# Performance work log

Measured on AMD Instinct MI355X. Metric: run time of the kernel, lower is better.

Reference implementation:

```python
import jax, jax.numpy as jnp
import numpy as np
from math import factorial

# ---- static config mirroring Cace.__init__ ----
MAX_L = 3            # max angular degree
N_RBF = 8            # Bessel radial basis size
RB = 8               # n_radial_basis (radial embedding dim after transform)
K = 3                # n_atom_basis -> edge channels C = K*K
NZ = 4               # len(zs)
CUTOFF = 5.5
N_NODES = 2000
N_EDGES = 50000
T_MP = 1             # num_message_passing
MP_NORM = 1.0 / np.sqrt(25.0)   # 1/sqrt(avg_num_neighbors)
C = K * K

def _lxlylz(max_l):
    out = []
    for l in range(max_l + 1):
        for lx in range(l, -1, -1):
            for ly in range(l - lx, -1, -1):
                out.append((lx, ly, l - lx - ly))
    return out

L_LIST = _lxlylz(MAX_L)                 # 20 Cartesian monomials for max_l=3
NL = len(L_LIST)
LX = np.array([t[0] for t in L_LIST]); LY = np.array([t[1] for t in L_LIST]); LZ = np.array([t[2] for t in L_LIST])
DEGS = LX + LY + LZ                     # degree l of each monomial
MULTI = np.array([factorial(int(d)) / (factorial(int(a)) * factorial(int(b)) * factorial(int(c)))
                  for a, b, c, d in zip(LX, LY, LZ, DEGS)], dtype=np.float32)
SEL = np.zeros((NL, MAX_L + 1), np.float32)
SEL[np.arange(NL), DEGS] = 1.0          # monomial -> degree one-hot (for per-l sums)
NB = 1 + (MAX_L + 1)                    # symmetrizer feats: nu=1 (l=0) + nu=2 per l

def bessel(r):  # [E] -> [E, N_RBF]
    n = jnp.arange(1, N_RBF + 1, dtype=r.dtype)
    return jnp.sqrt(2.0 / CUTOFF) * jnp.sin(n[None, :] * jnp.pi * r[:, None] / CUTOFF) / r[:, None]

def poly_cutoff(r):  # MACE-style polynomial cutoff, p=6
    p = 6.0
    u = r / CUTOFF
    f = 1.0 - (p + 1.0) * (p + 2.0) / 2.0 * u**6 + p * (p + 2.0) * u**7 - p * (p + 1.0) / 2.0 * u**8
    return f * (u < 1.0)

def axis_pows(x):  # [E] -> [E, MAX_L+1] = x^0..x^MAX_L (safe grads, handles negatives)
    pows = [jnp.ones_like(x)]
    for _ in range(MAX_L):
        pows.append(pows[-1] * x)
    return jnp.stack(pows, axis=1)

def angular(u):  # unit vectors [E,3] -> Cartesian monomials [E, NL]
    return axis_pows(u[:, 0])[:, LX] * axis_pows(u[:, 1])[:, LY] * axis_pows(u[:, 2])[:, LZ]

def radial_transform(x, W):  # x [N,R,L,C], W [MAX_L+1,R,Rb] shared per degree l
    return jnp.einsum('nrlc,lrb->nblc', x, W[DEGS])

def symmetrize(A):  # A [N,Rb,NL,C] -> B [N,Rb,NB,C]
    b1 = A[:, :, :1, :]  # nu=1: the (0,0,0) monomial (index 0)
    w = (A * A) * jnp.asarray(MULTI)[None, None, :, None]
    b2 = jnp.einsum('nrlc,lm->nrmc', w, jnp.asarray(SEL))  # nu=2 invariant per degree l
    return jnp.concatenate([b1, b2], axis=2)


def setup_inputs() -> dict:
    key = jax.random.key(0)
    ks = jax.random.split(key, 9)
    positions = jax.random.uniform(ks[0], (N_NODES, 3), dtype=jnp.float32) * 12.0
    species = jax.random.randint(ks[1], (N_NODES,), 0, NZ)
    send = jax.random.randint(ks[2], (N_EDGES,), 0, N_NODES)
    off = jax.random.randint(ks[3], (N_EDGES,), 1, N_NODES)
    recv = (send + off) % N_NODES  # no self-edges -> strictly positive edge lengths
    edge_index = jnp.stack([send, recv])
    shifts = jnp.zeros((N_EDGES, 3), jnp.float32)
    W_embed = jax.random.normal(ks[4], (NZ, K), jnp.float32)
    W_radial = jax.random.normal(ks[5], (MAX_L + 1, N_RBF, RB), jnp.float32) / np.sqrt(N_RBF)
    W_mem = jax.random.normal(ks[6], (MAX_L + 1, RB, RB), jnp.float32) / np.sqrt(RB)
    W_ar = jax.random.normal(ks[7], (N_RBF, RB), jnp.float32) / np.sqrt(N_RBF)
    W_chi = jax.random.normal(ks[8], (RB, NB), jnp.float32) * 0.1
    return {"positions": positions, "shifts": shifts, "W_embed": W_embed, "W_radial": W_radial,
            "W_mem": W_mem, "W_ar": W_ar, "W_chi": W_chi, "species": species, "edge_index": edge_index}


def reference(positions, shifts, W_embed, W_radial, W_mem, W_ar, W_chi, species, edge_index):
    n_nodes = positions.shape[0]
    send, recv = edge_index[0], edge_index[1]
    # edge geometry
    vec = positions[recv] - positions[send] + shifts
    lengths = jnp.linalg.norm(vec, axis=-1)
    u = vec / (lengths[:, None] + 1e-9)
    rad = bessel(lengths)          # [E,R]
    fcut = poly_cutoff(lengths)    # [E]
    ang = angular(u)               # [E,NL]
    # edge type encoding: outer product of sender/receiver species embeddings
    emb = W_embed[species]         # [N,K]
    enc = (emb[send][:, :, None] * emb[recv][:, None, :]).reshape(-1, C)  # [E,C]
    # elementwise_multiply_3tensors -> [E,R,NL,C]
    edge_attri = jnp.einsum('er,el,ec->erlc', rad * fcut[:, None], ang, enc)
    A = radial_transform(jax.ops.segment_sum(edge_attri, recv, num_segments=n_nodes), W_radial)  # [N,Rb,NL,C]
    B = symmetrize(A)              # [N,Rb,NB,C]
    feats = [B]
    for _ in range(T_MP):
        mem = jnp.einsum('nrlc,lrb->nblc', A, W_mem[DEGS])        # NodeMemory
        chi = jnp.einsum('nbkc,bk->nc', B, W_chi)                  # MessageBchi node scalar
        msg_bchi = edge_attri * chi[send][:, None, None, :]
        A_bchi = radial_transform(jax.ops.segment_sum(msg_bchi, recv, num_segments=n_nodes), W_radial)
        fr = (rad @ W_ar) * fcut[:, None]                          # MessageAr radial filter [E,Rb]
        msg_ar = A[send] * fr[:, :, None, None]
        A_ar = jax.ops.segment_sum(msg_ar, recv, num_segments=n_nodes)
        A = (A_ar + A_bchi) * MP_NORM + mem
        B = symmetrize(A)
        feats.append(B)
    return jnp.stack(feats, axis=-1)   # [N,Rb,NB,C,T_MP+1]
```

## Files before the change

kernel.cpp:

```cpp
#include <hip/hip_runtime.h>
#include <hip/hip_bf16.h>
#include <hip/hip_cooperative_groups.h>


#define CUTF 5.5f
#define MPNORM 0.2f

namespace cg = cooperative_groups;

__constant__ int   d_DEGS[20]  = {0,1,1,1,2,2,2,2,2,2,3,3,3,3,3,3,3,3,3,3};
__constant__ float d_MULTI[20] = {1,1,1,1,1,2,2,1,2,1,1,3,3,3,6,3,1,3,3,1};

__global__ __launch_bounds__(1024) void k_prep(const int* __restrict__ eidx,
                                               int* __restrict__ offs,
                                               int* __restrict__ cursor,
                                               int N, int E) {
  __shared__ int cnt[2048];
  __shared__ int part[1024];
  int t = threadIdx.x;
  cnt[t] = 0; cnt[t + 1024] = 0;
  for (int i = t; i < N; i += 1024) cursor[i] = 0;
  __syncthreads();
  const int* recv = eidx + E;
  if ((E & 3) == 0) {
    #pragma unroll 2
    for (int i = t * 4; i + 3 < E; i += 4096) {
      int4 v = *reinterpret_cast<const int4*>(recv + i);
      atomicAdd(&cnt[v.x], 1); atomicAdd(&cnt[v.y], 1);
      atomicAdd(&cnt[v.z], 1); atomicAdd(&cnt[v.w], 1);
    }
  } else {
    #pragma unroll 4
    for (int i = t; i < E; i += 1024) atomicAdd(&cnt[recv[i]], 1);
  }
  __syncthreads();
  int a = cnt[2 * t], b = cnt[2 * t + 1];
  int s = a + b;
  part[t] = s;
  __syncthreads();
  for (int d = 1; d < 1024; d <<= 1) {
    int add = (t >= d) ? part[t - d] : 0;
    __syncthreads();
    part[t] += add;
    __syncthreads();
  }
  int excl = part[t] - s;
  if (2 * t     < N) offs[2 * t]     = excl;
  if (2 * t + 1 < N) offs[2 * t + 1] = excl + a;
  if (t == 1023) offs[N] = part[1023];
}

__global__ void k_edge(const float* __restrict__ pos,
                       const float* __restrict__ shifts,
                       const float* __restrict__ Wemb,
                       const float* __restrict__ War,
                       const int* __restrict__ species,
                       const int* __restrict__ eidx,
                       const int* __restrict__ offs,
                       int* __restrict__ cursor,
                       float* __restrict__ edata,
                       int* __restrict__ esend,
                       int E) {
  __shared__ float war_s[64];
  int t = threadIdx.x;
  if (t < 64) war_s[t] = War[t];
  __syncthreads();
  int e = blockIdx.x * blockDim.x + t;
  if (e >= E) return;
  int s  = eidx[e];
  int rI = eidx[E + e];
  float vx = pos[rI*3+0] - pos[s*3+0] + shifts[e*3+0];
  float vy = pos[rI*3+1] - pos[s*3+1] + shifts[e*3+1];
  float vz = pos[rI*3+2] - pos[s*3+2] + shifts[e*3+2];
  float len = sqrtf(vx*vx + vy*vy + vz*vz);
  float inv = 1.0f / (len + 1e-9f);
  float ux = vx*inv, uy = vy*inv, uz = vz*inv;
  float uu = len * (1.0f/CUTF);
  float u2 = uu*uu, u6 = u2*u2*u2;
  float fcut = (uu < 1.0f) ? (1.0f - 28.0f*u6 + 48.0f*u6*uu - 21.0f*u6*u2) : 0.0f;
  float x = 3.14159265358979f * uu;
  float sn = sinf(x), c2 = 2.0f*cosf(x), snm1 = 0.0f;
  float pref = sqrtf(2.0f/CUTF) / (len + 1e-20f);
  float rad[8];
  float v[48];
  #pragma unroll
  for (int k = 0; k < 8; k++) {
    rad[k] = pref * sn;
    v[k]   = rad[k] * fcut;
    float nxt = c2*sn - snm1; snm1 = sn; sn = nxt;
  }
  #pragma unroll
  for (int b = 0; b < 8; b++) {
    float a = 0.0f;
    #pragma unroll
    for (int k = 0; k < 8; k++) a += rad[k] * war_s[k*8+b];
    v[8+b] = a * fcut;
  }
  float px2 = ux*ux, py2 = uy*uy, pz2 = uz*uz;
  v[16] = 1.0f; v[17] = ux;     v[18] = uy;     v[19] = uz;
  v[20] = px2;  v[21] = ux*uy;  v[22] = ux*uz;  v[23] = py2;
  v[24] = uy*uz;v[25] = pz2;
  v[26] = px2*ux; v[27] = px2*uy; v[28] = px2*uz; v[29] = ux*py2;
  v[30] = ux*uy*uz; v[31] = ux*pz2; v[32] = py2*uy; v[33] = py2*uz;
  v[34] = uy*pz2; v[35] = pz2*uz;
  int zs = species[s], zr = species[rI];
  float es0 = Wemb[zs*3+0], es1 = Wemb[zs*3+1], es2 = Wemb[zs*3+2];
  float er0 = Wemb[zr*3+0], er1 = Wemb[zr*3+1], er2 = Wemb[zr*3+2];
  v[36] = es0*er0; v[37] = es0*er1; v[38] = es0*er2;
  v[39] = es1*er0; v[40] = es1*er1; v[41] = es1*er2;
  v[42] = es2*er0; v[43] = es2*er1; v[44] = es2*er2;
  v[45] = 0.0f; v[46] = 0.0f; v[47] = 0.0f;
  int slot = atomicAdd(&cursor[rI], 1);
  int dst = offs[rI] + slot;
  float4* eb4 = reinterpret_cast<float4*>(edata + (size_t)dst * 48);
  #pragma unroll
  for (int w = 0; w < 12; w++)
    eb4[w] = make_float4(v[4*w], v[4*w+1], v[4*w+2], v[4*w+3]);
  esend[dst] = s;
}

__global__ __launch_bounds__(192, 3) void k_nodeF(
    const float* __restrict__ edata, const int* __restrict__ esend,
    const int* __restrict__ offs,
    const float* __restrict__ Wrad, const float* __restrict__ Wmem,
    const float* __restrict__ Wchi,
    uint4* __restrict__ Abf2, float* __restrict__ chi,
    float* __restrict__ out, int N, int G) {
  __shared__ float wr_s[288], wm_s[288];
  __shared__ float wchi_s[40];
  __shared__ float Bsh1[2][360];
  __shared__ float Bsh2[360];
  int t = threadIdx.x;
  for (int i = t; i < 256; i += 192) {
    int d = i >> 6, rm = i & 63;
    wr_s[d*72+rm] = Wrad[i];
    wm_s[d*72+rm] = Wmem[i];
  }
  for (int i = t; i < 40;  i += 192) wchi_s[i] = Wchi[i];
  for (int i = t; i < 720; i += 192) (&Bsh1[0][0])[i] = 0.0f;
  int l = t / 9, c = t - l*9;
  bool act = t < 180;
  int ll = act ? l : 0, cc = act ? c : 0;
  int tt = act ? t : 0;
  int deg = d_DEGS[ll];
  float mlt = d_MULTI[ll];
  int kk1 = 1 + deg;
  __syncthreads();

  float AbK[2][8];
  #pragma unroll
  for (int q = 0; q < 2; q++) {
    int n = blockIdx.x + q * G;
    if (n < N) {
      float acc[8];
      #pragma unroll
      for (int r = 0; r < 8; r++) acc[r] = 0.0f;
      int start = offs[n], end = offs[n+1];
      #pragma unroll 4
      for (int j = start; j < end; j++) {
        const float* row = edata + (size_t)j * 48;
        float p = row[16+ll] * row[36+cc];
        #pragma unroll
        for (int r = 0; r < 8; r++) acc[r] += row[r] * p;
      }
      const float* wp = &wr_s[deg*72];
      #pragma unroll
      for (int b = 0; b < 8; b++) {
        float a = 0.0f;
        #pragma unroll
        for (int r = 0; r < 8; r++) a += acc[r] * wp[r*8+b];
        AbK[q][b] = a;
      }
      if (act) {
        unsigned int pk[4];
        #pragma unroll
        for (int bp = 0; bp < 4; bp++) {
          __hip_bfloat16 blo = __float2bfloat16(AbK[q][2*bp]);
          __hip_bfloat16 bhi = __float2bfloat16(AbK[q][2*bp+1]);
          pk[bp] = (unsigned int)(*reinterpret_cast<unsigned short*>(&blo))
                 | ((unsigned int)(*reinterpret_cast<unsigned short*>(&bhi)) << 16);
        }
        uint4 qq; qq.x = pk[0]; qq.y = pk[1]; qq.z = pk[2]; qq.w = pk[3];
        Abf2[(size_t)n*180 + t] = qq;
        if (l == 0) {
          #pragma unroll
          for (int b = 0; b < 8; b++) Bsh1[q][b*45 + c] = AbK[q][b];
        }
        #pragma unroll
        for (int b = 0; b < 8; b++)
          atomicAdd(&Bsh1[q][b*45 + kk1*9 + c], mlt*AbK[q][b]*AbK[q][b]);
      }
    }
    __syncthreads();
    if (n < N && t < 9) {
      float s = 0.0f;
      for (int b = 0; b < 8; b++)
        #pragma unroll
        for (int kq = 0; kq < 5; kq++) s += Bsh1[q][b*45 + kq*9 + t] * wchi_s[b*5 + kq];
      chi[n*9 + t] = s;
    }
  }
  __threadfence();
  cg::this_grid().sync();
  #pragma unroll
  for (int q = 0; q < 2; q++) {
    int n = blockIdx.x + q * G;
    for (int i = t; i < 360; i += 192) Bsh2[i] = 0.0f;
    __syncthreads();
    if (n < N) {
      float Sacc[8], ARacc[8];
      #pragma unroll
      for (int r = 0; r < 8; r++) { Sacc[r] = 0.0f; ARacc[r] = 0.0f; }
      int start = offs[n], end = offs[n+1];
      #pragma unroll 4
      for (int j = start; j < end; j++) {
        const float* row = edata + (size_t)j * 48;
        int snd = esend[j];
        float ch = chi[snd*9 + cc];
        float pch = row[16+ll] * row[36+cc] * ch;
        #pragma unroll
        for (int r = 0; r < 8; r++) Sacc[r] += row[r] * pch;
        const uint4 qv = Abf2[(size_t)snd*180 + tt];
        float a0 = __uint_as_float(qv.x << 16), a1 = __uint_as_float(qv.x & 0xffff0000u);
        float a2 = __uint_as_float(qv.y << 16), a3 = __uint_as_float(qv.y & 0xffff0000u);
        float a4 = __uint_as_float(qv.z << 16), a5 = __uint_as_float(qv.z & 0xffff0000u);
        float a6 = __uint_as_float(qv.w << 16), a7 = __uint_as_float(qv.w & 0xffff0000u);
        ARacc[0] += a0*row[8];  ARacc[1] += a1*row[9];
        ARacc[2] += a2*row[10]; ARacc[3] += a3*row[11];
        ARacc[4] += a4*row[12]; ARacc[5] += a5*row[13];
        ARacc[6] += a6*row[14]; ARacc[7] += a7*row[15];
      }
      if (act) {
        const float* wrp = &wr_s[deg*72];
        const float* wmp = &wm_s[deg*72];
        float newA[8];
        #pragma unroll
        for (int b = 0; b < 8; b++) {
          float mem = 0.0f, ab = 0.0f;
          #pragma unroll
          for (int r = 0; r < 8; r++) { mem += AbK[q][r]*wmp[r*8+b]; ab += Sacc[r]*wrp[r*8+b]; }
          newA[b] = (ARacc[b] + ab)*MPNORM + mem;
        }
        if (l == 0) {
          #pragma unroll
          for (int b = 0; b < 8; b++) Bsh2[b*45 + c] = newA[b];
        }
        #pragma unroll
        for (int b = 0; b < 8; b++)
          atomicAdd(&Bsh2[b*45 + kk1*9 + c], mlt*newA[b]*newA[b]);
      }
    }
    __syncthreads();
    if (n < N) {
      float2* out2 = reinterpret_cast<float2*>(out);
      for (int i = t; i < 360; i += 192) {
        float2 pk2; pk2.x = Bsh1[q][i]; pk2.y = Bsh2[i];
        out2[(size_t)n*360 + i] = pk2;
      }
    }
    __syncthreads();
  }
}

__global__ __launch_bounds__(192) void k_nodeA(
    const float* __restrict__ edata, const int* __restrict__ offs,
    const float* __restrict__ Wrad, const float* __restrict__ Wchi,
    float* __restrict__ A, uint4* __restrict__ Abf2,
    float* __restrict__ chi, float* __restrict__ B0, int N) {
  __shared__ float wr_s[288];
  __shared__ float wchi_s[40];
  __shared__ float Bsh[360];
  int t = threadIdx.x, n = blockIdx.x;
  for (int i = t; i < 256; i += 192) { int d = i >> 6, rm = i & 63; wr_s[d*72+rm] = Wrad[i]; }
  for (int i = t; i < 40;  i += 192) wchi_s[i] = Wchi[i];
  for (int i = t; i < 360; i += 192) Bsh[i] = 0.0f;
  int l = t / 9, c = t - l*9;
  bool act = t < 180;
  int ll = act ? l : 0, cc = act ? c : 0;
  float acc[8];
  #pragma unroll
  for (int r = 0; r < 8; r++) acc[r] = 0.0f;
  int start = offs[n], end = offs[n+1];
  #pragma unroll 4
  for (int j = start; j < end; j++) {
    const float* row = edata + (size_t)j * 48;
    float p = row[16+ll] * row[36+cc];
    #pragma unroll
    for (int r = 0; r < 8; r++) acc[r] += row[r] * p;
  }
  __syncthreads();
  int deg = act ? d_DEGS[ll] : 0;
  const float* wp = &wr_s[deg*72];
  float Ab[8];
  #pragma unroll
  for (int b = 0; b < 8; b++) {
    float a = 0.0f;
    #pragma unroll
    for (int r = 0; r < 8; r++) a += acc[r] * wp[r*8+b];
    Ab[b] = a;
  }
  if (act) {
    #pragma unroll
    for (int b = 0; b < 8; b++) A[(size_t)n*1440 + t*8 + b] = Ab[b];
    unsigned int pk[4];
    #pragma unroll
    for (int bp = 0; bp < 4; bp++) {
      __hip_bfloat16 blo = __float2bfloat16(Ab[2*bp]);
      __hip_bfloat16 bhi = __float2bfloat16(Ab[2*bp+1]);
      pk[bp] = (unsigned int)(*reinterpret_cast<unsigned short*>(&blo))
             | ((unsigned int)(*reinterpret_cast<unsigned short*>(&bhi)) << 16);
    }
    uint4 qv; qv.x = pk[0]; qv.y = pk[1]; qv.z = pk[2]; qv.w = pk[3];
    Abf2[(size_t)n*180 + t] = qv;
    if (l == 0) {
      #pragma unroll
      for (int b = 0; b < 8; b++) Bsh[b*45 + c] = Ab[b];
    }
    float mlt = d_MULTI[ll]; int kk = 1 + deg;
    #pragma unroll
    for (int b = 0; b < 8; b++) atomicAdd(&Bsh[b*45 + kk*9 + c], mlt*Ab[b]*Ab[b]);
  }
  __syncthreads();
  if (t < 9) {
    float s = 0.0f;
    for (int b = 0; b < 8; b++)
      #pragma unroll
      for (int kq = 0; kq < 5; kq++) s += Bsh[b*45 + kq*9 + t] * wchi_s[b*5 + kq];
    chi[n*9 + t] = s;
  }
  for (int i = t; i < 360; i += 192)
    B0[(size_t)n*360 + i] = Bsh[i];
}

__global__ __launch_bounds__(192) void k_node2(
    const float* __restrict__ edata, const int* __restrict__ esend,
    const int* __restrict__ offs,
    const float* __restrict__ Wrad, const float* __restrict__ Wmem,
    const float* __restrict__ A, const uint4* __restrict__ Abf2,
    const float* __restrict__ chi, const float* __restrict__ B0,
    float* __restrict__ out, int N) {
  __shared__ float wr_s[288], wm_s[288];
  __shared__ float Bsh[360];
  int t = threadIdx.x, n = blockIdx.x;
  for (int i = t; i < 256; i += 192) {
    int d = i >> 6, rm = i & 63;
    wr_s[d*72+rm] = Wrad[i];
    wm_s[d*72+rm] = Wmem[i];
  }
  for (int i = t; i < 360; i += 192) Bsh[i] = 0.0f;
  int l = t / 9, c = t - l*9;
  bool act = t < 180;
  int ll = act ? l : 0, cc = act ? c : 0;
  int tt = act ? t : 0;
  float Sacc[8], ARacc[8];
  #pragma unroll
  for (int r = 0; r < 8; r++) { Sacc[r] = 0.0f; ARacc[r] = 0.0f; }
  int start = offs[n], end = offs[n+1];
  #pragma unroll 4
  for (int j = start; j < end; j++) {
    const float* row = edata + (size_t)j * 48;
    int snd = esend[j];
    float ch = chi[snd*9 + cc];
    float pch = row[16+ll] * row[36+cc] * ch;
    #pragma unroll
    for (int r = 0; r < 8; r++) Sacc[r] += row[r] * pch;
    const uint4 qv = Abf2[(size_t)snd*180 + tt];
    float a0 = __uint_as_float(qv.x << 16), a1 = __uint_as_float(qv.x & 0xffff0000u);
    float a2 = __uint_as_float(qv.y << 16), a3 = __uint_as_float(qv.y & 0xffff0000u);
    float a4 = __uint_as_float(qv.z << 16), a5 = __uint_as_float(qv.z & 0xffff0000u);
    float a6 = __uint_as_float(qv.w << 16), a7 = __uint_as_float(qv.w & 0xffff0000u);
    ARacc[0] += a0*row[8];  ARacc[1] += a1*row[9];
    ARacc[2] += a2*row[10]; ARacc[3] += a3*row[11];
    ARacc[4] += a4*row[12]; ARacc[5] += a5*row[13];
    ARacc[6] += a6*row[14]; ARacc[7] += a7*row[15];
  }
  __syncthreads();
  if (act) {
    int deg = d_DEGS[ll];
    const float* wrp = &wr_s[deg*72];
    const float* wmp = &wm_s[deg*72];
    const float* aop = A + (size_t)n*1440 + t*8;
    float aown[8];
    #pragma unroll
    for (int r = 0; r < 8; r++) aown[r] = aop[r];
    float newA[8];
    #pragma unroll
    for (int b = 0; b < 8; b++) {
      float mem = 0.0f, ab = 0.0f;
      #pragma unroll
      for (int r = 0; r < 8; r++) { mem += aown[r]*wmp[r*8+b]; ab += Sacc[r]*wrp[r*8+b]; }
      newA[b] = (ARacc[b] + ab)*MPNORM + mem;
    }
    if (l == 0) {
      #pragma unroll
      for (int b = 0; b < 8; b++) Bsh[b*45 + c] = newA[b];
    }
    float mlt = d_MULTI[ll]; int kk = 1 + deg;
    #pragma unroll
    for (int b = 0; b < 8; b++) atomicAdd(&Bsh[b*45 + kk*9 + c], mlt*newA[b]*newA[b]);
  }
  __syncthreads();
  float2* out2 = reinterpret_cast<float2*>(out);
  for (int i = t; i < 360; i += 192) {
    float2 pk; pk.x = B0[(size_t)n*360 + i]; pk.y = Bsh[i];
    out2[(size_t)n*360 + i] = pk;
  }
}

extern "C" void kernel_launch(void* const* d_in, const int* in_sizes, int n_in,
                              void* d_out, int out_size, void* d_ws, size_t ws_size,
                              hipStream_t stream) {
  const float* pos    = (const float*)d_in[0];
  const float* shifts = (const float*)d_in[1];
  const float* Wemb   = (const float*)d_in[2];
  const float* Wrad   = (const float*)d_in[3];
  const float* Wmem   = (const float*)d_in[4];
  const float* War    = (const float*)d_in[5];
  const float* Wchi   = (const float*)d_in[6];
  const int* species = (const int*)d_in[7];
  const int* eidx    = (const int*)d_in[8];
  float* out = (float*)d_out;
  int N = in_sizes[7];
  int E = in_sizes[8] / 2;

  char* base = (char*)d_ws;
  size_t off = 0;
  float* edata = (float*)(base + off); off += (size_t)E*48*4;
  float* A     = (float*)(base + off); off += (size_t)N*1440*4;
  uint4* Abf2  = (uint4*)(base + off); off += (size_t)N*180*16;
  float* chi   = (float*)(base + off); off += (size_t)N*9*4;
  float* B0    = (float*)(base + off); off += (size_t)N*360*4;
  int* cursor  = (int*)(base + off);   off += (size_t)N*4;
  int* offs    = (int*)(base + off);   off += (((size_t)(N+1)*4) + 15) & ~(size_t)15;
  int* esend   = (int*)(base + off);   off += (size_t)E*4;

  int G = (N + 1) / 2;

  static int s_coop = -1;
  static int s_G = 0;
  if (s_coop < 0) {
    int dev = 0; hipGetDevice(&dev);
    int nCU = 0;
    hipDeviceGetAttribute(&nCU, hipDeviceAttributeMultiprocessorCount, dev);
    int maxB = 0;
    hipError_t oe = hipOccupancyMaxActiveBlocksPerMultiprocessor(
        &maxB, reinterpret_cast<const void*>(k_nodeF), 192, 0);
    s_coop = (oe == hipSuccess && nCU > 0 && (long)maxB * nCU >= G) ? 1 : 0;
    s_G = G;
  }
  if (s_G != G) s_coop = 0;

  int eb = (E + 255) / 256;
  k_prep<<<1, 1024, 0, stream>>>(eidx, offs, cursor, N, E);
  k_edge<<<eb, 256, 0, stream>>>(pos, shifts, Wemb, War, species, eidx, offs, cursor,
                                 edata, esend, E);

  bool done = false;
  if (s_coop == 1) {
    void* args[] = {(void*)&edata, (void*)&esend, (void*)&offs,
                    (void*)&Wrad, (void*)&Wmem, (void*)&Wchi,
                    (void*)&Abf2, (void*)&chi, (void*)&out,
                    (void*)&N, (void*)&G};
    hipError_t le = hipLaunchCooperativeKernel(
        reinterpret_cast<void*>(k_nodeF), dim3(G), dim3(192), args, 0, stream);
    if (le == hipSuccess) done = true; else s_coop = 0;
  }
  if (!done) {
    k_nodeA<<<N, 192, 0, stream>>>(edata, offs, Wrad, Wchi, A, Abf2, chi, B0, N);
    k_node2<<<N, 192, 0, stream>>>(edata, esend, offs, Wrad, Wmem, A, Abf2, chi, B0, out, N);
  }
}
```

Before: 152.0 us.

## Split CSR build into parallel count/scan and use one node per cooperative block

Replaces the single-block histogram+scan prep kernel with a grid-wide atomic count kernel that records each edge's rank, followed by a small 256-thread scan. The edge kernel then places rows from the precomputed rank instead of doing its own atomic cursor increment, and runs with 64-thread blocks. The cooperative node kernel now processes one node per block with a grid of N blocks and launch bounds raised to 6 blocks per CU, dropping the two-nodes-per-block loop. The aim is more parallelism in the serial prep phase and in the node phase. The cost is extra launches and a memset, plus reliance on enough co-resident blocks for the cooperative launch, otherwise it falls back to the two-kernel path.

```diff
diff --git a/kernel.cpp b/kernel.cpp
--- a/kernel.cpp
+++ b/kernel.cpp
@@ -11,64 +11,59 @@
 __constant__ int   d_DEGS[20]  = {0,1,1,1,2,2,2,2,2,2,3,3,3,3,3,3,3,3,3,3};
 __constant__ float d_MULTI[20] = {1,1,1,1,1,2,2,1,2,1,1,3,3,3,6,3,1,3,3,1};
 
-__global__ __launch_bounds__(1024) void k_prep(const int* __restrict__ eidx,
-                                               int* __restrict__ offs,
-                                               int* __restrict__ cursor,
-                                               int N, int E) {
-  __shared__ int cnt[2048];
-  __shared__ int part[1024];
+__global__ void k_count(const int* __restrict__ eidx, int* __restrict__ counts,
+                        int* __restrict__ erank, int E) {
+  int e = blockIdx.x * blockDim.x + threadIdx.x;
+  if (e < E) erank[e] = atomicAdd(&counts[eidx[E + e]], 1);
+}
+
+__global__ void k_scan(const int* __restrict__ counts, int* __restrict__ offs, int N) {
+  __shared__ int part[256];
   int t = threadIdx.x;
-  cnt[t] = 0; cnt[t + 1024] = 0;
-  for (int i = t; i < N; i += 1024) cursor[i] = 0;
-  __syncthreads();
-  const int* recv = eidx + E;
-  if ((E & 3) == 0) {
-    #pragma unroll 2
-    for (int i = t * 4; i + 3 < E; i += 4096) {
-      int4 v = *reinterpret_cast<const int4*>(recv + i);
-      atomicAdd(&cnt[v.x], 1); atomicAdd(&cnt[v.y], 1);
-      atomicAdd(&cnt[v.z], 1); atomicAdd(&cnt[v.w], 1);
-    }
-  } else {
-    #pragma unroll 4
-    for (int i = t; i < E; i += 1024) atomicAdd(&cnt[recv[i]], 1);
-  }
-  __syncthreads();
-  int a = cnt[2 * t], b = cnt[2 * t + 1];
-  int s = a + b;
-  part[t] = s;
-  __syncthreads();
-  for (int d = 1; d < 1024; d <<= 1) {
-    int add = (t >= d) ? part[t - d] : 0;
+  int local[8]; int sum = 0;
+  #pragma unroll
+  for (int i = 0; i < 8; i++) {
+    int idx = t*8 + i;
+    int v = (idx < N) ? counts[idx] : 0;
+    local[i] = sum; sum += v;
+  }
+  part[t] = sum; __syncthreads();
+  for (int d = 1; d < 256; d <<= 1) {
+    int add = (t >= d) ? part[t-d] : 0;
     __syncthreads();
     part[t] += add;
     __syncthreads();
   }
-  int excl = part[t] - s;
-  if (2 * t     < N) offs[2 * t]     = excl;
-  if (2 * t + 1 < N) offs[2 * t + 1] = excl + a;
-  if (t == 1023) offs[N] = part[1023];
-}
-
-__global__ void k_edge(const float* __restrict__ pos,
+  int excl = part[t] - sum;
+  #pragma unroll
+  for (int i = 0; i < 8; i++) {
+    int idx = t*8 + i;
+    if (idx < N) offs[idx] = excl + local[i];
+  }
+  if (t == 255) offs[N] = part[255];
+}
+
+__global__ __launch_bounds__(64) void k_edge(
+                       const float* __restrict__ pos,
                        const float* __restrict__ shifts,
                        const float* __restrict__ Wemb,
                        const float* __restrict__ War,
                        const int* __restrict__ species,
                        const int* __restrict__ eidx,
                        const int* __restrict__ offs,
-                       int* __restrict__ cursor,
+                       const int* __restrict__ erank,
                        float* __restrict__ edata,
                        int* __restrict__ esend,
                        int E) {
   __shared__ float war_s[64];
   int t = threadIdx.x;
-  if (t < 64) war_s[t] = War[t];
-  __syncthreads();
-  int e = blockIdx.x * blockDim.x + t;
+  war_s[t] = War[t];
+  __syncthreads();
+  int e = blockIdx.x * 64 + t;
   if (e >= E) return;
   int s  = eidx[e];
   int rI = eidx[E + e];
+  int rk = erank[e];
   float vx = pos[rI*3+0] - pos[s*3+0] + shifts[e*3+0];
   float vy = pos[rI*3+1] - pos[s*3+1] + shifts[e*3+1];
   float vz = pos[rI*3+2] - pos[s*3+2] + shifts[e*3+2];
@@ -110,8 +105,7 @@
   v[39] = es1*er0; v[40] = es1*er1; v[41] = es1*er2;
   v[42] = es2*er0; v[43] = es2*er1; v[44] = es2*er2;
   v[45] = 0.0f; v[46] = 0.0f; v[47] = 0.0f;
-  int slot = atomicAdd(&cursor[rI], 1);
-  int dst = offs[rI] + slot;
+  int dst = offs[rI] + rk;
   float4* eb4 = reinterpret_cast<float4*>(edata + (size_t)dst * 48);
   #pragma unroll
   for (int w = 0; w < 12; w++)
@@ -119,146 +113,124 @@
   esend[dst] = s;
 }
 
-__global__ __launch_bounds__(192, 3) void k_nodeF(
+__global__ __launch_bounds__(192, 6) void k_nodeF(
     const float* __restrict__ edata, const int* __restrict__ esend,
     const int* __restrict__ offs,
     const float* __restrict__ Wrad, const float* __restrict__ Wmem,
     const float* __restrict__ Wchi,
     uint4* __restrict__ Abf2, float* __restrict__ chi,
-    float* __restrict__ out, int N, int G) {
+    float* __restrict__ out, int N) {
   __shared__ float wr_s[288], wm_s[288];
   __shared__ float wchi_s[40];
-  __shared__ float Bsh1[2][360];
-  __shared__ float Bsh2[360];
-  int t = threadIdx.x;
+  __shared__ float Bsh1[360], Bsh2[360];
+  int t = threadIdx.x, n = blockIdx.x;
   for (int i = t; i < 256; i += 192) {
     int d = i >> 6, rm = i & 63;
     wr_s[d*72+rm] = Wrad[i];
     wm_s[d*72+rm] = Wmem[i];
   }
   for (int i = t; i < 40;  i += 192) wchi_s[i] = Wchi[i];
-  for (int i = t; i < 720; i += 192) (&Bsh1[0][0])[i] = 0.0f;
+  for (int i = t; i < 360; i += 192) { Bsh1[i] = 0.0f; Bsh2[i] = 0.0f; }
   int l = t / 9, c = t - l*9;
   bool act = t < 180;
   int ll = act ? l : 0, cc = act ? c : 0;
   int tt = act ? t : 0;
   int deg = d_DEGS[ll];
   float mlt = d_MULTI[ll];
-  int kk1 = 1 + deg;
-  __syncthreads();
-
-  float AbK[2][8];
-  #pragma unroll
-  for (int q = 0; q < 2; q++) {
-    int n = blockIdx.x + q * G;
-    if (n < N) {
-      float acc[8];
-      #pragma unroll
-      for (int r = 0; r < 8; r++) acc[r] = 0.0f;
-      int start = offs[n], end = offs[n+1];
-      #pragma unroll 4
-      for (int j = start; j < end; j++) {
-        const float* row = edata + (size_t)j * 48;
-        float p = row[16+ll] * row[36+cc];
-        #pragma unroll
-        for (int r = 0; r < 8; r++) acc[r] += row[r] * p;
-      }
-      const float* wp = &wr_s[deg*72];
-      #pragma unroll
-      for (int b = 0; b < 8; b++) {
-        float a = 0.0f;
-        #pragma unroll
-        for (int r = 0; r < 8; r++) a += acc[r] * wp[r*8+b];
-        AbK[q][b] = a;
-      }
-      if (act) {
-        unsigned int pk[4];
-        #pragma unroll
-        for (int bp = 0; bp < 4; bp++) {
-          __hip_bfloat16 blo = __float2bfloat16(AbK[q][2*bp]);
-          __hip_bfloat16 bhi = __float2bfloat16(AbK[q][2*bp+1]);
-          pk[bp] = (unsigned int)(*reinterpret_cast<unsigned short*>(&blo))
-                 | ((unsigned int)(*reinterpret_cast<unsigned short*>(&bhi)) << 16);
-        }
-        uint4 qq; qq.x = pk[0]; qq.y = pk[1]; qq.z = pk[2]; qq.w = pk[3];
-        Abf2[(size_t)n*180 + t] = qq;
-        if (l == 0) {
-          #pragma unroll
-          for (int b = 0; b < 8; b++) Bsh1[q][b*45 + c] = AbK[q][b];
-        }
-        #pragma unroll
-        for (int b = 0; b < 8; b++)
-          atomicAdd(&Bsh1[q][b*45 + kk1*9 + c], mlt*AbK[q][b]*AbK[q][b]);
-      }
-    }
-    __syncthreads();
-    if (n < N && t < 9) {
-      float s = 0.0f;
-      for (int b = 0; b < 8; b++)
-        #pragma unroll
-        for (int kq = 0; kq < 5; kq++) s += Bsh1[q][b*45 + kq*9 + t] * wchi_s[b*5 + kq];
-      chi[n*9 + t] = s;
-    }
+  int kk = 1 + deg;
+  int start = offs[n], end = offs[n+1];
+  __syncthreads();
+  float acc[8];
+  #pragma unroll
+  for (int r = 0; r < 8; r++) acc[r] = 0.0f;
+  #pragma unroll 4
+  for (int j = start; j < end; j++) {
+    const float* row = edata + (size_t)j * 48;
+    float p = row[16+ll] * row[36+cc];
+    #pragma unroll
+    for (int r = 0; r < 8; r++) acc[r] += row[r] * p;
+  }
+  const float* wp = &wr_s[deg*72];
+  float Ab[8];
+  #pragma unroll
+  for (int b = 0; b < 8; b++) {
+    float a = 0.0f;
+    #pragma unroll
+    for (int r = 0; r < 8; r++) a += acc[r] * wp[r*8+b];
+    Ab[b] = a;
+  }
+  if (act) {
+    unsigned int pk[4];
+    #pragma unroll
+    for (int bp = 0; bp < 4; bp++) {
+      __hip_bfloat16 blo = __float2bfloat16(Ab[2*bp]);
+      __hip_bfloat16 bhi = __float2bfloat16(Ab[2*bp+1]);
+      pk[bp] = (unsigned int)(*reinterpret_cast<unsigned short*>(&blo))
+             | ((unsigned int)(*reinterpret_cast<unsigned short*>(&bhi)) << 16);
+    }
+    uint4 qv; qv.x = pk[0]; qv.y = pk[1]; qv.z = pk[2]; qv.w = pk[3];
+    Abf2[(size_t)n*180 + t] = qv;
+    if (l == 0) {
+      #pragma unroll
+      for (int b = 0; b < 8; b++) Bsh1[b*45 + c] = Ab[b];
+    }
+    #pragma unroll
+    for (int b = 0; b < 8; b++) atomicAdd(&Bsh1[b*45 + kk*9 + c], mlt*Ab[b]*Ab[b]);
+  }
+  __syncthreads();
+  if (t < 9) {
+    float s = 0.0f;
+    for (int b = 0; b < 8; b++)
+      #pragma unroll
+      for (int kq = 0; kq < 5; kq++) s += Bsh1[b*45 + kq*9 + t] * wchi_s[b*5 + kq];
+    chi[n*9 + t] = s;
   }
   __threadfence();
   cg::this_grid().sync();
-  #pragma unroll
-  for (int q = 0; q < 2; q++) {
-    int n = blockIdx.x + q * G;
-    for (int i = t; i < 360; i += 192) Bsh2[i] = 0.0f;
-    __syncthreads();
-    if (n < N) {
-      float Sacc[8], ARacc[8];
-      #pragma unroll
-      for (int r = 0; r < 8; r++) { Sacc[r] = 0.0f; ARacc[r] = 0.0f; }
-      int start = offs[n], end = offs[n+1];
-      #pragma unroll 4
-      for (int j = start; j < end; j++) {
-        const float* row = edata + (size_t)j * 48;
-        int snd = esend[j];
-        float ch = chi[snd*9 + cc];
-        float pch = row[16+ll] * row[36+cc] * ch;
-        #pragma unroll
-        for (int r = 0; r < 8; r++) Sacc[r] += row[r] * pch;
-        const uint4 qv = Abf2[(size_t)snd*180 + tt];
-        float a0 = __uint_as_float(qv.x << 16), a1 = __uint_as_float(qv.x & 0xffff0000u);
-        float a2 = __uint_as_float(qv.y << 16), a3 = __uint_as_float(qv.y & 0xffff0000u);
-        float a4 = __uint_as_float(qv.z << 16), a5 = __uint_as_float(qv.z & 0xffff0000u);
-        float a6 = __uint_as_float(qv.w << 16), a7 = __uint_as_float(qv.w & 0xffff0000u);
-        ARacc[0] += a0*row[8];  ARacc[1] += a1*row[9];
-        ARacc[2] += a2*row[10]; ARacc[3] += a3*row[11];
-        ARacc[4] += a4*row[12]; ARacc[5] += a5*row[13];
-        ARacc[6] += a6*row[14]; ARacc[7] += a7*row[15];
-      }
-      if (act) {
-        const float* wrp = &wr_s[deg*72];
-        const float* wmp = &wm_s[deg*72];
-        float newA[8];
-        #pragma unroll
-        for (int b = 0; b < 8; b++) {
-          float mem = 0.0f, ab = 0.0f;
-          #pragma unroll
-          for (int r = 0; r < 8; r++) { mem += AbK[q][r]*wmp[r*8+b]; ab += Sacc[r]*wrp[r*8+b]; }
-          newA[b] = (ARacc[b] + ab)*MPNORM + mem;
-        }
-        if (l == 0) {
-          #pragma unroll
-          for (int b = 0; b < 8; b++) Bsh2[b*45 + c] = newA[b];
-        }
-        #pragma unroll
-        for (int b = 0; b < 8; b++)
-          atomicAdd(&Bsh2[b*45 + kk1*9 + c], mlt*newA[b]*newA[b]);
-      }
-    }
-    __syncthreads();
-    if (n < N) {
-      float2* out2 = reinterpret_cast<float2*>(out);
-      for (int i = t; i < 360; i += 192) {
-        float2 pk2; pk2.x = Bsh1[q][i]; pk2.y = Bsh2[i];
-        out2[(size_t)n*360 + i] = pk2;
-      }
-    }
-    __syncthreads();
+  float Sacc[8], Racc[8];
+  #pragma unroll
+  for (int r = 0; r < 8; r++) { Sacc[r] = 0.0f; Racc[r] = 0.0f; }
+  #pragma unroll 2
+  for (int j = start; j < end; j++) {
+    const float* row = edata + (size_t)j * 48;
+    int snd = esend[j];
+    float ch = chi[snd*9 + cc];
+    const uint4 qv = Abf2[(size_t)snd*180 + tt];
+    float pch = row[16+ll] * row[36+cc] * ch;
+    #pragma unroll
+    for (int r = 0; r < 8; r++) Sacc[r] += row[r] * pch;
+    float a0 = __uint_as_float(qv.x << 16), a1 = __uint_as_float(qv.x & 0xffff0000u);
+    float a2 = __uint_as_float(qv.y << 16), a3 = __uint_as_float(qv.y & 0xffff0000u);
+    float a4 = __uint_as_float(qv.z << 16), a5 = __uint_as_float(qv.z & 0xffff0000u);
+    float a6 = __uint_as_float(qv.w << 16), a7 = __uint_as_float(qv.w & 0xffff0000u);
+    Racc[0] += a0*row[8];  Racc[1] += a1*row[9];
+    Racc[2] += a2*row[10]; Racc[3] += a3*row[11];
+    Racc[4] += a4*row[12]; Racc[5] += a5*row[13];
+    Racc[6] += a6*row[14]; Racc[7] += a7*row[15];
+  }
+  if (act) {
+    const float* wrp = &wr_s[deg*72];
+    const float* wmp = &wm_s[deg*72];
+    float newA[8];
+    #pragma unroll
+    for (int b = 0; b < 8; b++) {
+      float mem = 0.0f, ab = 0.0f;
+      #pragma unroll
+      for (int r = 0; r < 8; r++) { mem += Ab[r]*wmp[r*8+b]; ab += Sacc[r]*wrp[r*8+b]; }
+      newA[b] = (Racc[b] + ab)*MPNORM + mem;
+    }
+    if (l == 0) {
+      #pragma unroll
+      for (int b = 0; b < 8; b++) Bsh2[b*45 + c] = newA[b];
+    }
+    #pragma unroll
+    for (int b = 0; b < 8; b++) atomicAdd(&Bsh2[b*45 + kk*9 + c], mlt*newA[b]*newA[b]);
+  }
+  __syncthreads();
+  float2* out2 = reinterpret_cast<float2*>(out);
+  for (int i = t; i < 360; i += 192) {
+    float2 pk2; pk2.x = Bsh1[i]; pk2.y = Bsh2[i];
+    out2[(size_t)n*360 + i] = pk2;
   }
 }
 
@@ -430,39 +402,37 @@
   uint4* Abf2  = (uint4*)(base + off); off += (size_t)N*180*16;
   float* chi   = (float*)(base + off); off += (size_t)N*9*4;
   float* B0    = (float*)(base + off); off += (size_t)N*360*4;
-  int* cursor  = (int*)(base + off);   off += (size_t)N*4;
+  int* counts  = (int*)(base + off);   off += (size_t)N*4;
   int* offs    = (int*)(base + off);   off += (((size_t)(N+1)*4) + 15) & ~(size_t)15;
   int* esend   = (int*)(base + off);   off += (size_t)E*4;
-
-  int G = (N + 1) / 2;
+  int* erank   = (int*)(base + off);   off += (((size_t)E*4) + 15) & ~(size_t)15;
 
   static int s_coop = -1;
-  static int s_G = 0;
-  if (s_coop < 0) {
+  static int s_N = 0;
+  if (s_coop < 0 || s_N != N) {
     int dev = 0; hipGetDevice(&dev);
     int nCU = 0;
     hipDeviceGetAttribute(&nCU, hipDeviceAttributeMultiprocessorCount, dev);
     int maxB = 0;
     hipError_t oe = hipOccupancyMaxActiveBlocksPerMultiprocessor(
         &maxB, reinterpret_cast<const void*>(k_nodeF), 192, 0);
-    s_coop = (oe == hipSuccess && nCU > 0 && (long)maxB * nCU >= G) ? 1 : 0;
-    s_G = G;
-  }
-  if (s_G != G) s_coop = 0;
-
-  int eb = (E + 255) / 256;
-  k_prep<<<1, 1024, 0, stream>>>(eidx, offs, cursor, N, E);
-  k_edge<<<eb, 256, 0, stream>>>(pos, shifts, Wemb, War, species, eidx, offs, cursor,
-                                 edata, esend, E);
+    s_coop = (oe == hipSuccess && nCU > 0 && (long)maxB * nCU >= N) ? 1 : 0;
+    s_N = N;
+  }
+
+  hipMemsetAsync(counts, 0, (size_t)N*4, stream);
+  k_count<<<(E + 255) / 256, 256, 0, stream>>>(eidx, counts, erank, E);
+  k_scan<<<1, 256, 0, stream>>>(counts, offs, N);
+  k_edge<<<(E + 63) / 64, 64, 0, stream>>>(pos, shifts, Wemb, War, species, eidx,
+                                           offs, erank, edata, esend, E);
 
   bool done = false;
   if (s_coop == 1) {
     void* args[] = {(void*)&edata, (void*)&esend, (void*)&offs,
                     (void*)&Wrad, (void*)&Wmem, (void*)&Wchi,
-                    (void*)&Abf2, (void*)&chi, (void*)&out,
-                    (void*)&N, (void*)&G};
+                    (void*)&Abf2, (void*)&chi, (void*)&out, (void*)&N};
     hipError_t le = hipLaunchCooperativeKernel(
-        reinterpret_cast<void*>(k_nodeF), dim3(G), dim3(192), args, 0, stream);
+        reinterpret_cast<void*>(k_nodeF), dim3(N), dim3(192), args, 0, stream);
     if (le == hipSuccess) done = true; else s_coop = 0;
   }
   if (!done) {
```

Result: no change. 153.6 us (+1.0%).
